# Kernel optimization log

Hardware: AMD Instinct MI355X
Metric: run time of the kernel (lower is better)

The kernel has to match this reference:

```python
import jax, jax.numpy as jnp
import numpy as np

LOW_RANK = 32      # low_rank_dim
N_CAND = 2048      # n_candidates
CHUNK = 128        # chunk_size
AUX_PCT = 0.2      # Settings.aux_loss_percent


def _normalize(x, eps=1e-12):
    # matches torch.nn.functional.normalize(p=2, dim=-1)
    n = jnp.linalg.norm(x, axis=-1, keepdims=True)
    return x / jnp.maximum(n, eps)


def setup_inputs() -> dict:
    key = jax.random.key(0)
    k1, k2, k3 = jax.random.split(key, 3)
    V, D, B, S = 50257, 1024, 4, 2048
    return {
        "hidden_states": jax.random.normal(k1, (B, S, D), jnp.float32),
        "embedding_weight": jax.random.normal(k2, (V, D), jnp.float32) * 0.02,
        "logit_scale": jnp.asarray(2.6592, jnp.float32),
        "target_ids": jax.random.randint(k3, (B, S), 0, V, dtype=jnp.int32),
    }


def reference(hidden_states, embedding_weight, logit_scale, target_ids):
    d = hidden_states.shape[-1]
    h = hidden_states.reshape(-1, d)            # [T, d]
    t = target_ids.reshape(-1)                  # [T]
    T = h.shape[0]
    n_chunks = T // CHUNK                       # T assumed divisible by CHUNK

    # no_grad low-rank table used only for candidate scan
    w_low_norm = jax.lax.stop_gradient(_normalize(embedding_weight[:, :LOW_RANK]))  # [V, L]
    h_low = _normalize(h[:, :LOW_RANK]).reshape(n_chunks, CHUNK, LOW_RANK)          # [n, C, L]
    h_full = _normalize(h).reshape(n_chunks, CHUNK, d)                              # [n, C, d]
    t_c = t.reshape(n_chunks, CHUNK)

    scale = 100.0 * jax.nn.sigmoid(logit_scale) + 1.0

    # with_batch_mean=True path: one scan per chunk using chunk-mean query (no_grad)
    h_mean = jax.lax.stop_gradient(h_low.mean(axis=1))      # [n, L]
    scan_logits = h_mean @ w_low_norm.T                     # [n, V]
    _, top_idx = jax.lax.top_k(scan_logits, N_CAND)         # [n, K]

    cand = embedding_weight[top_idx]                        # [n, K, d] (gather)
    cand_n = _normalize(cand)
    full_sims = jnp.einsum('ncd,nkd->nck', h_full, cand_n)  # [n, C, K]

    w_low_cand = _normalize(cand[..., :LOW_RANK])           # [n, K, L]
    low_sims = jnp.einsum('ncl,nkl->nck', h_low, w_low_cand)

    tgt_emb = embedding_weight[t_c]                         # [n, C, d]
    tgt_full_sim = jnp.sum(h_full * _normalize(tgt_emb), axis=-1)              # [n, C]
    tgt_low_sim = jnp.sum(h_low * _normalize(tgt_emb[..., :LOW_RANK]), axis=-1)

    is_tgt = top_idx[:, None, :] == t_c[:, :, None]         # [n, C, K]
    neg_inf = jnp.float32(-jnp.inf)

    # cross_entropy with label 0 == logsumexp(logits) - logits[..., 0]
    main_logits = jnp.concatenate(
        [tgt_full_sim[..., None] * scale,
         jnp.where(is_tgt, neg_inf, full_sims * scale)], axis=-1)
    main_loss = jnp.sum(jax.nn.logsumexp(main_logits, axis=-1) - main_logits[..., 0])

    aux_logits = jnp.concatenate(
        [tgt_low_sim[..., None] * scale,
         jnp.where(is_tgt, neg_inf, low_sims * scale)], axis=-1)
    aux_loss = jnp.sum(jax.nn.logsumexp(aux_logits, axis=-1) - aux_logits[..., 0])

    return (main_loss + AUX_PCT * aux_loss) / T
```

## Files before the change

### kernel.cpp

```cpp
#include <hip/hip_runtime.h>
#include <cstdint>
#include <cstddef>

#define V_SIZE 50257
#define V_PAD  50432
#define NV4    (V_PAD/4)
#define NVB    ((V_SIZE + 3) / 4)
#define D_DIM  1024
#define T_TOK  8192
#define NCHUNK 64
#define CCHUNK 128
#define NCAND  2048
#define LOWR   32
#define SDCAP  4096
#define ESCALE 32.0f

typedef unsigned int  uint32;
typedef unsigned short u16;
typedef unsigned char u8;
typedef unsigned long long u64;
typedef __attribute__((ext_vector_type(8))) short short8;
typedef __attribute__((ext_vector_type(4))) float f32x4;

__device__ __forceinline__ u16 f2bf(float f){
  uint32 u = __float_as_uint(f);
  return (u16)((u + 0x7FFFu + ((u >> 16) & 1u)) >> 16);
}
__device__ __forceinline__ uint32 key_of(float f){
  uint32 b = __float_as_uint(f);
  return b ^ ((uint32)((int)b >> 31) | 0x80000000u);
}
__device__ __forceinline__ int fxbin(float x){
  float c = fmaxf(fminf(x, 0.49f), -0.49f);
  int b = (int)(c * 4096.f) + 1024;
  return b < 0 ? 0 : (b > 2047 ? 2047 : b);
}
__device__ __forceinline__ float sigscale(const float* lsc){
  return 100.f / (1.f + __expf(-lsc[0])) + 1.f;
}
__device__ __forceinline__ float wred_sum(float v){
  #pragma unroll
  for (int m = 32; m >= 1; m >>= 1) v += __shfl_xor(v, m, 64);
  return v;
}
__device__ __forceinline__ float wred_max(float v){
  #pragma unroll
  for (int m = 32; m >= 1; m >>= 1) v = fmaxf(v, __shfl_xor(v, m, 64));
  return v;
}
__device__ __forceinline__ void gload_lds16(const void* g, void* l){
  __builtin_amdgcn_global_load_lds(
      (const __attribute__((address_space(1))) uint32*)g,
      (__attribute__((address_space(3))) uint32*)l, 16, 0, 0);
}
__device__ __forceinline__ void load_row16(const float* base, int lane, float* f){
  const float4* s4 = (const float4*)(base + lane * 16);
  float4 t0 = s4[0], t1 = s4[1], t2 = s4[2], t3 = s4[3];
  f[0]=t0.x; f[1]=t0.y; f[2]=t0.z;  f[3]=t0.w;
  f[4]=t1.x; f[5]=t1.y; f[6]=t1.z;  f[7]=t1.w;
  f[8]=t2.x; f[9]=t2.y; f[10]=t2.z; f[11]=t2.w;
  f[12]=t3.x; f[13]=t3.y; f[14]=t3.z; f[15]=t3.w;
}
__device__ __forceinline__ void store_bf16x16(u16* dst_base, int lane, const float* f){
  uint32 pk[8];
  #pragma unroll
  for (int i=0;i<8;++i) pk[i] = (uint32)f2bf(f[2*i]) | ((uint32)f2bf(f[2*i+1]) << 16);
  uint4* d = (uint4*)(dst_base + lane * 16);
  d[0] = make_uint4(pk[0],pk[1],pk[2],pk[3]);
  d[1] = make_uint4(pk[4],pk[5],pk[6],pk[7]);
}
__device__ __forceinline__ void store_fp8x16(u8* dst_base, int lane, const float* f, float sc){
  uint32 pk[4];
  #pragma unroll
  for (int i=0;i<4;++i){
    int w = __builtin_amdgcn_cvt_pk_fp8_f32(f[4*i]*sc,   f[4*i+1]*sc, 0, false);
    w     = __builtin_amdgcn_cvt_pk_fp8_f32(f[4*i+2]*sc, f[4*i+3]*sc, w, true);
    pk[i] = (uint32)w;
  }
  *(uint4*)(dst_base + lane * 16) = make_uint4(pk[0],pk[1],pk[2],pk[3]);
}
__device__ __forceinline__ int a8(int r, int slot8){
  return r*64 + ((((slot8>>1) ^ (r&3))) << 4) + ((slot8&1) << 3);
}

__global__ void __launch_bounds__(256)
prep_kernel(const float* __restrict__ emb, u8* __restrict__ emb8,
            u16* __restrict__ elow16,
            float* __restrict__ invn_f, float* __restrict__ invn_l,
            float* __restrict__ wlow,
            const float* __restrict__ h, u8* __restrict__ h8,
            u16* __restrict__ hlow16,
            float* __restrict__ invh_f, float* __restrict__ invh_l,
            float* __restrict__ hpart, uint32* __restrict__ ghist,
            float* __restrict__ out)
{
  const int bid = blockIdx.x;
  const int tid = threadIdx.x, lane = tid & 63, wid = tid >> 6;
  if (bid < NVB){
    if (bid == 0 && tid == 0) out[0] = 0.f;
    if (bid < 512 && tid < 64)
      ((uint4*)ghist)[bid * 64 + tid] = make_uint4(0,0,0,0);
    const int v = bid * 4 + wid;
    if (v >= V_SIZE) return;
    float f[16];
    load_row16(emb + (size_t)v * D_DIM, lane, f);
    float ss = 0.f;
    #pragma unroll
    for (int k=0;k<16;++k) ss += f[k]*f[k];
    float fullss = wred_sum(ss);
    float lowss  = wred_sum(lane < 2 ? ss : 0.f);
    store_fp8x16(emb8 + (size_t)v * D_DIM, lane, f, ESCALE);
    if (lane < 2){
      store_bf16x16(elow16 + (size_t)v * LOWR, lane, f);
      float4* wp = (float4*)(wlow + (size_t)v * LOWR + lane * 16);
      wp[0] = make_float4(f[0], f[1], f[2],  f[3]);
      wp[1] = make_float4(f[4], f[5], f[6],  f[7]);
      wp[2] = make_float4(f[8], f[9], f[10], f[11]);
      wp[3] = make_float4(f[12],f[13],f[14], f[15]);
    }
    if (lane == 0){
      invn_f[v] = 1.f / fmaxf(sqrtf(fullss), 1e-12f);
      invn_l[v] = 1.f / fmaxf(sqrtf(lowss),  1e-12f);
    }
    return;
  }
  const int bid2 = bid - NVB;
  const int nchunk = bid2 >> 3, sub = bid2 & 7;
  __shared__ float hm[LOWR];
  if (tid < LOWR) hm[tid] = 0.f;
  __syncthreads();
  for (int i = 0; i < 4; ++i){
    const int loc = sub*16 + wid*4 + i;
    const int tok = nchunk * CCHUNK + loc;
    float f[16];
    load_row16(h + (size_t)tok * D_DIM, lane, f);
    float ss = 0.f;
    #pragma unroll
    for (int k=0;k<16;++k) ss += f[k]*f[k];
    float fullss = wred_sum(ss);
    float lowss  = wred_sum(lane < 2 ? ss : 0.f);
    float invf = 1.f / fmaxf(sqrtf(fullss), 1e-12f);
    float invl = 1.f / fmaxf(sqrtf(lowss),  1e-12f);
    store_fp8x16(h8 + (size_t)tok * D_DIM, lane, f, 1.0f);
    if (lane < 2) store_bf16x16(hlow16 + (size_t)tok * LOWR, lane, f);
    if (lane == 0){ invh_f[tok] = invf; invh_l[tok] = invl; }
    if (lane < 2){
      #pragma unroll
      for (int k=0;k<16;++k) atomicAdd(&hm[lane*16 + k], f[k] * invl * (1.f/128.f));
    }
  }
  __syncthreads();
  if (tid < LOWR) hpart[(size_t)(nchunk*8 + sub) * LOWR + tid] = hm[tid];
}

__global__ void __launch_bounds__(256)
scan_kernel(const float* __restrict__ wlow, const float* __restrict__ invn_l,
            const float* __restrict__ hpart, float* __restrict__ scan)
{
  __shared__ float hm[NCHUNK * LOWR];
  for (int i = threadIdx.x; i < NCHUNK * LOWR; i += 256){
    const int nn = i >> 5, l = i & 31;
    float s = 0.f;
    #pragma unroll
    for (int p = 0; p < 8; ++p) s += hpart[(size_t)(nn*8 + p) * LOWR + l];
    hm[i] = s;
  }
  __syncthreads();
  const int v = blockIdx.x * 256 + threadIdx.x;
  if (v >= V_SIZE){
    if (v < V_PAD)
      for (int nn = 0; nn < NCHUNK; ++nn) scan[(size_t)nn * V_PAD + v] = -3.4e38f;
    return;
  }
  float w[LOWR];
  const float4* s4 = (const float4*)(wlow + (size_t)v * LOWR);
  #pragma unroll
  for (int i=0;i<8;++i){
    float4 t = s4[i];
    w[4*i]=t.x; w[4*i+1]=t.y; w[4*i+2]=t.z; w[4*i+3]=t.w;
  }
  const float inv = invn_l[v];
  #pragma unroll
  for (int i=0;i<LOWR;++i) w[i] *= inv;
  for (int nn = 0; nn < NCHUNK; ++nn){
    float d = 0.f;
    #pragma unroll
    for (int l=0;l<LOWR;++l) d += w[l] * hm[nn*LOWR + l];
    scan[(size_t)nn * V_PAD + v] = d;
  }
}

__global__ void __launch_bounds__(256)
topk_hist(const float* __restrict__ scan, uint32* __restrict__ ghist)
{
  const int nchunk = blockIdx.x, sub = blockIdx.y, tid = threadIdx.x;
  __shared__ uint32 hh[4][2048];
  for (int i = tid; i < 4*2048; i += 256) (&hh[0][0])[i] = 0;
  __syncthreads();
  const int cp = (tid >> 6) & 3;
  const float4* row = (const float4*)(scan + (size_t)nchunk * V_PAD) + sub * (NV4/8);
  for (int i = tid; i < NV4/8; i += 256){
    float4 x = row[i];
    atomicAdd(&hh[cp][fxbin(x.x)], 1u);
    atomicAdd(&hh[cp][fxbin(x.y)], 1u);
    atomicAdd(&hh[cp][fxbin(x.z)], 1u);
    atomicAdd(&hh[cp][fxbin(x.w)], 1u);
  }
  __syncthreads();
  uint32* gh = ghist + nchunk * 2048;
  for (int i = tid; i < 2048; i += 256){
    uint32 s = hh[0][i] + hh[1][i] + hh[2][i] + hh[3][i];
    if (s) atomicAdd(&gh[i], s);
  }
}

__global__ void __launch_bounds__(1024)
topk_select(const float* __restrict__ scan, const uint32* __restrict__ ghist,
            const float* __restrict__ invn_f, const float* __restrict__ invn_l,
            int* __restrict__ topidx, float* __restrict__ invc_f, float* __restrict__ invc_l)
{
  const int nchunk = blockIdx.x, tid = threadIdx.x, lane = tid & 63;
  __shared__ uint32 h[2048];
  __shared__ int gt_list[2048];
  __shared__ u64 sd_list[SDCAP];
  __shared__ uint32 rh[256];
  __shared__ uint32 n_gt, n_sd, s_tb, s_cgt, s_sel, s_cum, s_pos;
  if (tid == 0){ n_gt = 0; n_sd = 0; s_pos = 0; }
  for (int i = tid; i < 2048; i += 1024) h[i] = ghist[nchunk * 2048 + i];
  __syncthreads();
  if (tid < 64){
    uint32 c = 0;
    #pragma unroll 8
    for (int k = 0; k < 32; ++k) c += h[lane*32 + k];
    uint32 s = c;
    #pragma unroll
    for (int off = 1; off < 64; off <<= 1){
      uint32 t = __shfl_down(s, off, 64);
      if (lane + off < 64) s += t;
    }
    u64 m1 = __ballot(s >= NCAND);
    const int g = 63 - __builtin_clzll(m1);
    const uint32 cum = (g < 63) ? __shfl(s, g + 1, 64) : 0u;
    uint32 s2 = (lane < 32) ? h[g*32 + lane] : 0u;
    #pragma unroll
    for (int off = 1; off < 32; off <<= 1){
      uint32 t = __shfl_down(s2, off, 64);
      if (lane + off < 32) s2 += t;
    }
    u64 m2 = __ballot((lane < 32) && (cum + s2 >= NCAND));
    const int j = 63 - __builtin_clzll(m2);
    const uint32 cgt = cum + ((j < 31) ? __shfl(s2, j + 1, 64) : 0u);
    if (lane == 0){ s_tb = (uint32)(g*32 + j); s_cgt = cgt; }
  }
  __syncthreads();
  const int tb = (int)s_tb;
  const uint32 cgt = s_cgt;
  const float4* row = (const float4*)(scan + (size_t)nchunk * V_PAD);
  for (int i = tid; i < NV4; i += 1024){
    float4 x = row[i];
    const int vbase = i * 4;
    float vals[4] = {x.x, x.y, x.z, x.w};
    #pragma unroll
    for (int c = 0; c < 4; ++c){
      const int b = fxbin(vals[c]);
      const int v = vbase + c;
      const bool ok = (v < V_SIZE) && (b >= tb);
      const bool is_gt = ok && (b > tb);
      const bool is_sd = ok && (b == tb);
      const u64 mg = __ballot(is_gt);
      if (mg){
        const int ldr = (int)__builtin_ctzll(mg);
        uint32 base = 0;
        if (lane == ldr) base = atomicAdd(&n_gt, (uint32)__popcll(mg));
        base = __shfl(base, ldr, 64);
        if (is_gt){
          uint32 p = base + (uint32)__popcll(mg & ((1ull << lane) - 1ull));
          if (p < 2048u) gt_list[p] = v;
        }
      }
      const u64 ms = __ballot(is_sd);
      if (ms){
        const int ldr = (int)__builtin_ctzll(ms);
        uint32 base = 0;
        if (lane == ldr) base = atomicAdd(&n_sd, (uint32)__popcll(ms));
        base = __shfl(base, ldr, 64);
        if (is_sd){
          uint32 p = base + (uint32)__popcll(ms & ((1ull << lane) - 1ull));
          if (p < (uint32)SDCAP)
            sd_list[p] = ((u64)(~key_of(vals[c])) << 32) | (uint32)v;
        }
      }
    }
  }
  __syncthreads();
  const uint32 ng = n_gt < 2048u ? n_gt : 2048u;
  for (uint32 i = tid; i < ng; i += 1024){
    const int v = gt_list[i];
    const int o = nchunk * NCAND + (int)i;
    topidx[o] = v; invc_f[o] = invn_f[v]; invc_l[o] = invn_l[v];
  }
  const int n = (int)(n_sd < (uint32)SDCAP ? n_sd : (uint32)SDCAP);
  uint32 r = NCAND - cgt; if ((int)r > n) r = (uint32)n;
  u64 pref = 0;
  uint32 rem = r;
  const int bytes6[6] = {7,6,5,4,1,0};
  for (int bi = 0; bi < 6; ++bi){
    const int by = bytes6[bi];
    if (tid < 256) rh[tid] = 0;
    __syncthreads();
    const u64 pmask = (by == 7) ? 0ull : ((~0ull) << ((by+1)*8));
    for (int i = tid; i < n; i += 1024){
      u64 x = sd_list[i];
      if ((x & pmask) == pref) atomicAdd(&rh[(uint32)(x >> (by*8)) & 255u], 1u);
    }
    __syncthreads();
    if (tid < 64){
      const uint32 b0 = rh[lane*4], b1 = rh[lane*4+1], b2 = rh[lane*4+2], b3 = rh[lane*4+3];
      uint32 ps = b0 + b1 + b2 + b3;
      #pragma unroll
      for (int off = 1; off < 64; off <<= 1){
        uint32 t = __shfl_up(ps, off, 64);
        if (lane >= off) ps += t;
      }
      const u64 mm = __ballot(ps >= rem);
      const int gl = (int)__builtin_ctzll(mm);
      const uint32 before = (gl > 0) ? __shfl(ps, gl-1, 64) : 0u;
      if (lane == gl){
        uint32 cum = before; uint32 bsel = (uint32)gl * 4;
        if (cum + b0 < rem){ cum += b0; bsel++;
          if (cum + b1 < rem){ cum += b1; bsel++;
            if (cum + b2 < rem){ cum += b2; bsel++; } } }
        s_sel = bsel; s_cum = cum;
      }
    }
    __syncthreads();
    pref |= ((u64)s_sel) << (by*8);
    rem -= s_cum;
    __syncthreads();
  }
  for (int i = tid; i < n; i += 1024){
    u64 x = sd_list[i];
    if (x <= pref){
      uint32 p = atomicAdd(&s_pos, 1u);
      const int v = (int)(uint32)x;
      const int o = nchunk * NCAND + (int)(cgt + p);
      topidx[o] = v; invc_f[o] = invn_f[v]; invc_l[o] = invn_l[v];
    }
  }
}

__global__ void __launch_bounds__(256)
gemm_fused(const u8* __restrict__ h8, const u8* __restrict__ emb8,
           const u16* __restrict__ hlow16, const u16* __restrict__ elow16,
           const int* __restrict__ topidx,
           const float* __restrict__ invh_f, const float* __restrict__ invc_f,
           const float* __restrict__ invh_l, const float* __restrict__ invc_l,
           const int* __restrict__ tgts, const float* __restrict__ lsc,
           float* __restrict__ pm, float* __restrict__ pa)
{
  constexpr int NSTEP = 16;
  const int id = blockIdx.x;
  const int s_ = id >> 3;
  const int ntile = s_ & 31;
  const int nchunk = ((s_ >> 5) << 3) | (id & 7);
  const int tid = threadIdx.x, lane = tid & 63, wid = tid >> 6;
  const int wm = wid;
  const int fq = lane >> 4, fr = lane & 15;

  __shared__ u8 As[CCHUNK * 64];
  __shared__ u8 Bs[64 * 64];
  __shared__ float s_invh[CCHUNK], s_invhl[CCHUNK];
  __shared__ float s_invc[64], s_invcl[64];
  __shared__ int   s_tgt[CCHUNK], s_idx[64];

  if (tid < CCHUNK){
    s_invh[tid]  = invh_f[nchunk * CCHUNK + tid];
    s_invhl[tid] = invh_l[nchunk * CCHUNK + tid];
    s_tgt[tid]   = tgts[nchunk * CCHUNK + tid];
  }
  if (tid < 64){
    int o = nchunk * NCAND + ntile * 64 + tid;
    s_idx[tid]  = topidx[o];
    s_invc[tid] = invc_f[o];
    s_invcl[tid] = invc_l[o];
  }

  const int rl = lane >> 2;
  const int cbyte = ((lane & 3) ^ (rl & 3)) * 16;
  const char* aptr[2];
  const char* alptr[2];
  const char* bptr;
  const char* blptr;
  #pragma unroll
  for (int s = 0; s < 2; ++s){
    int row = wid * 32 + s * 16 + rl;
    aptr[s]  = (const char*)h8 + ((size_t)(nchunk * CCHUNK + row)) * D_DIM + cbyte;
    alptr[s] = (const char*)hlow16 + ((size_t)(nchunk * CCHUNK + row)) * (LOWR*2) + cbyte;
  }
  {
    int brow = wid * 16 + rl;
    int cidx = topidx[nchunk * NCAND + ntile * 64 + brow];
    bptr  = (const char*)emb8 + (size_t)cidx * D_DIM + cbyte;
    blptr = (const char*)elow16 + (size_t)cidx * (LOWR*2) + cbyte;
  }

  f32x4 acc[2][4];
  #pragma unroll
  for (int m=0;m<2;++m)
    #pragma unroll
    for (int q=0;q<4;++q)
      acc[m][q] = (f32x4){0.f,0.f,0.f,0.f};

  for (int st = 0; st < NSTEP; ++st){
    const int koff = st * 64;
    gload_lds16(aptr[0] + koff, (void*)&As[(wid*32 + 0 ) * 64]);
    gload_lds16(aptr[1] + koff, (void*)&As[(wid*32 + 16) * 64]);
    gload_lds16(bptr + koff,    (void*)&Bs[(wid*16) * 64]);
    __syncthreads();
    #pragma unroll
    for (int kk = 0; kk < 2; ++kk){
      long af[2], bf[4];
      #pragma unroll
      for (int m=0;m<2;++m)
        af[m] = *(const long*)&As[a8(wm*32 + m*16 + fr, kk*4 + fq)];
      #pragma unroll
      for (int q=0;q<4;++q)
        bf[q] = *(const long*)&Bs[a8(q*16 + fr, kk*4 + fq)];
      #pragma unroll
      for (int m=0;m<2;++m)
        #pragma unroll
        for (int q=0;q<4;++q)
          acc[m][q] = __builtin_amdgcn_mfma_f32_16x16x32_fp8_fp8(af[m], bf[q], acc[m][q], 0, 0, 0);
    }
    __syncthreads();
  }

  gload_lds16(alptr[0], (void*)&As[(wid*32 + 0 ) * 64]);
  gload_lds16(alptr[1], (void*)&As[(wid*32 + 16) * 64]);
  gload_lds16(blptr,    (void*)&Bs[(wid*16) * 64]);

  const float scale = sigscale(lsc);
  const float scm = scale * (1.0f / ESCALE);
  const float NEG = -__builtin_huge_valf();

  #pragma unroll
  for (int m=0;m<2;++m){
    #pragma unroll
    for (int j=0;j<4;++j){
      const int c = wm*32 + m*16 + fq*4 + j;
      const float ihs = s_invh[c] * scm;
      const int tg = s_tgt[c];
      float vals[4];
      #pragma unroll
      for (int q=0;q<4;++q){
        const int kl = q*16 + fr;
        float lg = acc[m][q][j] * ihs * s_invc[kl];
        vals[q] = (s_idx[kl] == tg) ? NEG : lg;
      }
      float lmax = fmaxf(fmaxf(vals[0], vals[1]), fmaxf(vals[2], vals[3]));
      #pragma unroll
      for (int ms=1; ms<16; ms<<=1) lmax = fmaxf(lmax, __shfl_xor(lmax, ms, 64));
      float se = 0.f;
      #pragma unroll
      for (int q=0;q<4;++q) se += __expf(vals[q] - lmax);
      #pragma unroll
      for (int ms=1; ms<16; ms<<=1) se += __shfl_xor(se, ms, 64);
      if (fr == 0){
        size_t pos = ((size_t)(nchunk*32 + ntile) * CCHUNK + c) * 2;
        pm[pos]   = lmax;
        pm[pos+1] = se;
      }
    }
  }

  __syncthreads();

  f32x4 acc2[2][4];
  {
    short8 afa[2], bfa[4];
    #pragma unroll
    for (int m=0;m<2;++m){
      const int r = wm*32 + m*16 + fr;
      afa[m] = *(const short8*)&As[r*64 + ((fq ^ (r & 3)) << 4)];
    }
    #pragma unroll
    for (int q=0;q<4;++q){
      const int r = q*16 + fr;
      bfa[q] = *(const short8*)&Bs[r*64 + ((fq ^ (r & 3)) << 4)];
    }
    #pragma unroll
    for (int m=0;m<2;++m)
      #pragma unroll
      for (int q=0;q<4;++q)
        acc2[m][q] = __builtin_amdgcn_mfma_f32_16x16x32_bf16(
            afa[m], bfa[q], (f32x4){0.f,0.f,0.f,0.f}, 0, 0, 0);
  }

  #pragma unroll
  for (int m=0;m<2;++m){
    #pragma unroll
    for (int j=0;j<4;++j){
      const int c = wm*32 + m*16 + fq*4 + j;
      const float ihs = s_invhl[c] * scale;
      const int tg = s_tgt[c];
      float vals[4];
      #pragma unroll
      for (int q=0;q<4;++q){
        const int kl = q*16 + fr;
        float lg = acc2[m][q][j] * ihs * s_invcl[kl];
        vals[q] = (s_idx[kl] == tg) ? NEG : lg;
      }
      float lmax = fmaxf(fmaxf(vals[0], vals[1]), fmaxf(vals[2], vals[3]));
      #pragma unroll
      for (int ms=1; ms<16; ms<<=1) lmax = fmaxf(lmax, __shfl_xor(lmax, ms, 64));
      float se = 0.f;
      #pragma unroll
      for (int q=0;q<4;++q) se += __expf(vals[q] - lmax);
      #pragma unroll
      for (int ms=1; ms<16; ms<<=1) se += __shfl_xor(se, ms, 64);
      if (fr == 0){
        size_t pos = ((size_t)(nchunk*32 + ntile) * CCHUNK + c) * 2;
        pa[pos]   = lmax;
        pa[pos+1] = se;
      }
    }
  }
}

__global__ void __launch_bounds__(256)
merge_loss(const float* __restrict__ h, const float* __restrict__ emb,
           const int* __restrict__ tgts,
           const float* __restrict__ invh_f, const float* __restrict__ invh_l,
           const float* __restrict__ invn_f, const float* __restrict__ invn_l,
           const float* __restrict__ pm, const float* __restrict__ pa,
           const float* __restrict__ lsc, float* __restrict__ out)
{
  const int nchunk = blockIdx.x >> 2, quarter = blockIdx.x & 3;
  const int tid = threadIdx.x, lane = tid & 63, wid = tid >> 6;
  const float scale = sigscale(lsc);
  const float NEG = -__builtin_huge_valf();
  float wacc = 0.f;
  for (int i = 0; i < 8; ++i){
    const int loc = quarter*32 + wid*8 + i;
    const int tok = nchunk * CCHUNK + loc;
    const int t = tgts[tok];
    float hf[16], ef[16];
    load_row16(h + (size_t)tok * D_DIM, lane, hf);
    load_row16(emb + (size_t)t * D_DIM, lane, ef);
    float part = 0.f;
    #pragma unroll
    for (int k=0;k<16;++k) part += hf[k]*ef[k];
    float dfull = wred_sum(part);
    float dlow  = wred_sum(lane < 2 ? part : 0.f);
    float tful = dfull * invh_f[tok] * invn_f[t] * scale;
    float tlow = dlow  * invh_l[tok] * invn_l[t] * scale;

    float mi = NEG, si = 0.f, mia = NEG, sia = 0.f;
    if (lane < 32){
      size_t q = ((size_t)(nchunk*32 + lane) * CCHUNK + loc) * 2;
      mi  = pm[q]; si  = pm[q+1];
      mia = pa[q]; sia = pa[q+1];
    }
    float M  = wred_max(mi);
    float S  = wred_sum(lane < 32 ? si * __expf(mi - M) : 0.f);
    float M2 = fmaxf(M, tful);
    float lmain = __logf(S * __expf(M - M2) + __expf(tful - M2)) + M2 - tful;
    float Ma  = wred_max(mia);
    float Sa  = wred_sum(lane < 32 ? sia * __expf(mia - Ma) : 0.f);
    float M2a = fmaxf(Ma, tlow);
    float laux = __logf(Sa * __expf(Ma - M2a) + __expf(tlow - M2a)) + M2a - tlow;
    wacc += lmain + 0.2f * laux;
  }
  __shared__ float ws4[4];
  if (lane == 0) ws4[wid] = wacc;
  __syncthreads();
  if (tid == 0) atomicAdd(out, (ws4[0]+ws4[1]+ws4[2]+ws4[3]) * (1.f / (float)T_TOK));
}

extern "C" void kernel_launch(void* const* d_in, const int* in_sizes, int n_in,
                              void* d_out, int out_size, void* d_ws, size_t ws_size,
                              hipStream_t stream)
{
  (void)in_sizes; (void)n_in; (void)out_size; (void)ws_size;
  const float* h   = (const float*)d_in[0];
  const float* emb = (const float*)d_in[1];
  const float* lsc = (const float*)d_in[2];
  const int*   tgt = (const int*)d_in[3];
  float* out = (float*)d_out;

  uint8_t* p = (uint8_t*)d_ws;
  auto carve = [&](size_t n)->uint8_t*{
    uint8_t* r = p; p += (n + 255) & ~(size_t)255; return r;
  };
  u8*    emb8   = (u8*)   carve((size_t)V_SIZE * D_DIM);
  u16*   elow16 = (u16*)  carve((size_t)V_SIZE * LOWR * 2);
  float* invn_f = (float*)carve((size_t)V_SIZE * 4);
  float* invn_l = (float*)carve((size_t)V_SIZE * 4);
  float* wlow   = (float*)carve((size_t)V_SIZE * LOWR * 4);
  u8*    h8     = (u8*)   carve((size_t)T_TOK * D_DIM);
  u16*   hlow16 = (u16*)  carve((size_t)T_TOK * LOWR * 2);
  float* invh_f = (float*)carve((size_t)T_TOK * 4);
  float* invh_l = (float*)carve((size_t)T_TOK * 4);
  float* hpart  = (float*)carve((size_t)NCHUNK * 8 * LOWR * 4);
  float* scan   = (float*)carve((size_t)NCHUNK * V_PAD * 4);
  uint32* ghist = (uint32*)carve((size_t)NCHUNK * 2048 * 4);
  int*   topidx = (int*)  carve((size_t)NCHUNK * NCAND * 4);
  float* invc_f = (float*)carve((size_t)NCHUNK * NCAND * 4);
  float* invc_l = (float*)carve((size_t)NCHUNK * NCAND * 4);
  float* pm     = (float*)carve((size_t)NCHUNK * 32 * CCHUNK * 2 * 4);
  float* pa     = (float*)carve((size_t)NCHUNK * 32 * CCHUNK * 2 * 4);

  prep_kernel<<<dim3(NVB + NCHUNK*8), dim3(256), 0, stream>>>(
      emb, emb8, elow16, invn_f, invn_l, wlow, h, h8, hlow16,
      invh_f, invh_l, hpart, ghist, out);
  scan_kernel<<<dim3(V_PAD / 256), dim3(256), 0, stream>>>(wlow, invn_l, hpart, scan);
  topk_hist<<<dim3(NCHUNK, 8), dim3(256), 0, stream>>>(scan, ghist);
  topk_select<<<dim3(NCHUNK), dim3(1024), 0, stream>>>(
      scan, ghist, invn_f, invn_l, topidx, invc_f, invc_l);
  gemm_fused<<<dim3(32 * NCHUNK), dim3(256), 0, stream>>>(
      h8, emb8, hlow16, elow16, topidx, invh_f, invc_f, invh_l, invc_l, tgt, lsc, pm, pa);
  merge_loss<<<dim3(NCHUNK * 4), dim3(256), 0, stream>>>(
      h, emb, tgt, invh_f, invh_l, invn_f, invn_l, pm, pa, lsc, out);
}
```

Baseline: 187.6 us.

## Fuse top-k histogram into select kernel and spread merge_loss over more blocks

Merges the separate histogram and selection kernels into a single per-chunk kernel that builds the bin histogram in shared memory. This removes the global histogram buffer, its zeroing in prep, the global atomics and one launch. The cost is that each chunk's histogram is now built by one 1024-thread block (64 blocks total) instead of 512 blocks, so there is less parallelism for that pass. merge_loss also goes from 256 to 1024 blocks, each handling 8 tokens, to raise occupancy at the price of more atomic adds to the output.

```diff
diff --git a/kernel.cpp b/kernel.cpp
--- a/kernel.cpp
+++ b/kernel.cpp
@@ -91,15 +91,12 @@
             const float* __restrict__ h, u8* __restrict__ h8,
             u16* __restrict__ hlow16,
             float* __restrict__ invh_f, float* __restrict__ invh_l,
-            float* __restrict__ hpart, uint32* __restrict__ ghist,
-            float* __restrict__ out)
+            float* __restrict__ hpart, float* __restrict__ out)
 {
   const int bid = blockIdx.x;
   const int tid = threadIdx.x, lane = tid & 63, wid = tid >> 6;
   if (bid < NVB){
     if (bid == 0 && tid == 0) out[0] = 0.f;
-    if (bid < 512 && tid < 64)
-      ((uint4*)ghist)[bid * 64 + tid] = make_uint4(0,0,0,0);
     const int v = bid * 4 + wid;
     if (v >= V_SIZE) return;
     float f[16];
@@ -190,16 +187,23 @@
   }
 }
 
-__global__ void __launch_bounds__(256)
-topk_hist(const float* __restrict__ scan, uint32* __restrict__ ghist)
+__global__ void __launch_bounds__(1024)
+topk_all(const float* __restrict__ scan,
+         const float* __restrict__ invn_f, const float* __restrict__ invn_l,
+         int* __restrict__ topidx, float* __restrict__ invc_f, float* __restrict__ invc_l)
 {
-  const int nchunk = blockIdx.x, sub = blockIdx.y, tid = threadIdx.x;
+  const int nchunk = blockIdx.x, tid = threadIdx.x, lane = tid & 63;
   __shared__ uint32 hh[4][2048];
-  for (int i = tid; i < 4*2048; i += 256) (&hh[0][0])[i] = 0;
-  __syncthreads();
+  __shared__ int gt_list[2048];
+  __shared__ u64 sd_list[SDCAP];
+  __shared__ uint32 rh[256];
+  __shared__ uint32 n_gt, n_sd, s_tb, s_cgt, s_sel, s_cum, s_pos;
+  if (tid == 0){ n_gt = 0; n_sd = 0; s_pos = 0; }
+  for (int i = tid; i < 4*2048; i += 1024) (&hh[0][0])[i] = 0;
+  __syncthreads();
+  const float4* row = (const float4*)(scan + (size_t)nchunk * V_PAD);
   const int cp = (tid >> 6) & 3;
-  const float4* row = (const float4*)(scan + (size_t)nchunk * V_PAD) + sub * (NV4/8);
-  for (int i = tid; i < NV4/8; i += 256){
+  for (int i = tid; i < NV4; i += 1024){
     float4 x = row[i];
     atomicAdd(&hh[cp][fxbin(x.x)], 1u);
     atomicAdd(&hh[cp][fxbin(x.y)], 1u);
@@ -207,31 +211,13 @@
     atomicAdd(&hh[cp][fxbin(x.w)], 1u);
   }
   __syncthreads();
-  uint32* gh = ghist + nchunk * 2048;
-  for (int i = tid; i < 2048; i += 256){
-    uint32 s = hh[0][i] + hh[1][i] + hh[2][i] + hh[3][i];
-    if (s) atomicAdd(&gh[i], s);
-  }
-}
-
-__global__ void __launch_bounds__(1024)
-topk_select(const float* __restrict__ scan, const uint32* __restrict__ ghist,
-            const float* __restrict__ invn_f, const float* __restrict__ invn_l,
-            int* __restrict__ topidx, float* __restrict__ invc_f, float* __restrict__ invc_l)
-{
-  const int nchunk = blockIdx.x, tid = threadIdx.x, lane = tid & 63;
-  __shared__ uint32 h[2048];
-  __shared__ int gt_list[2048];
-  __shared__ u64 sd_list[SDCAP];
-  __shared__ uint32 rh[256];
-  __shared__ uint32 n_gt, n_sd, s_tb, s_cgt, s_sel, s_cum, s_pos;
-  if (tid == 0){ n_gt = 0; n_sd = 0; s_pos = 0; }
-  for (int i = tid; i < 2048; i += 1024) h[i] = ghist[nchunk * 2048 + i];
+  for (int i = tid; i < 2048; i += 1024)
+    hh[0][i] = hh[0][i] + hh[1][i] + hh[2][i] + hh[3][i];
   __syncthreads();
   if (tid < 64){
     uint32 c = 0;
     #pragma unroll 8
-    for (int k = 0; k < 32; ++k) c += h[lane*32 + k];
+    for (int k = 0; k < 32; ++k) c += hh[0][lane*32 + k];
     uint32 s = c;
     #pragma unroll
     for (int off = 1; off < 64; off <<= 1){
@@ -241,7 +227,7 @@
     u64 m1 = __ballot(s >= NCAND);
     const int g = 63 - __builtin_clzll(m1);
     const uint32 cum = (g < 63) ? __shfl(s, g + 1, 64) : 0u;
-    uint32 s2 = (lane < 32) ? h[g*32 + lane] : 0u;
+    uint32 s2 = (lane < 32) ? hh[0][g*32 + lane] : 0u;
     #pragma unroll
     for (int off = 1; off < 32; off <<= 1){
       uint32 t = __shfl_down(s2, off, 64);
@@ -255,7 +241,6 @@
   __syncthreads();
   const int tb = (int)s_tb;
   const uint32 cgt = s_cgt;
-  const float4* row = (const float4*)(scan + (size_t)nchunk * V_PAD);
   for (int i = tid; i < NV4; i += 1024){
     float4 x = row[i];
     const int vbase = i * 4;
@@ -535,13 +520,13 @@
            const float* __restrict__ pm, const float* __restrict__ pa,
            const float* __restrict__ lsc, float* __restrict__ out)
 {
-  const int nchunk = blockIdx.x >> 2, quarter = blockIdx.x & 3;
+  const int nchunk = blockIdx.x >> 4, sixteenth = blockIdx.x & 15;
   const int tid = threadIdx.x, lane = tid & 63, wid = tid >> 6;
   const float scale = sigscale(lsc);
   const float NEG = -__builtin_huge_valf();
   float wacc = 0.f;
-  for (int i = 0; i < 8; ++i){
-    const int loc = quarter*32 + wid*8 + i;
+  for (int i = 0; i < 2; ++i){
+    const int loc = sixteenth*8 + wid*2 + i;
     const int tok = nchunk * CCHUNK + loc;
     const int t = tgts[tok];
     float hf[16], ef[16];
@@ -603,7 +588,6 @@
   float* invh_l = (float*)carve((size_t)T_TOK * 4);
   float* hpart  = (float*)carve((size_t)NCHUNK * 8 * LOWR * 4);
   float* scan   = (float*)carve((size_t)NCHUNK * V_PAD * 4);
-  uint32* ghist = (uint32*)carve((size_t)NCHUNK * 2048 * 4);
   int*   topidx = (int*)  carve((size_t)NCHUNK * NCAND * 4);
   float* invc_f = (float*)carve((size_t)NCHUNK * NCAND * 4);
   float* invc_l = (float*)carve((size_t)NCHUNK * NCAND * 4);
@@ -612,13 +596,12 @@
 
   prep_kernel<<<dim3(NVB + NCHUNK*8), dim3(256), 0, stream>>>(
       emb, emb8, elow16, invn_f, invn_l, wlow, h, h8, hlow16,
-      invh_f, invh_l, hpart, ghist, out);
+      invh_f, invh_l, hpart, out);
   scan_kernel<<<dim3(V_PAD / 256), dim3(256), 0, stream>>>(wlow, invn_l, hpart, scan);
-  topk_hist<<<dim3(NCHUNK, 8), dim3(256), 0, stream>>>(scan, ghist);
-  topk_select<<<dim3(NCHUNK), dim3(1024), 0, stream>>>(
-      scan, ghist, invn_f, invn_l, topidx, invc_f, invc_l);
+  topk_all<<<dim3(NCHUNK), dim3(1024), 0, stream>>>(
+      scan, invn_f, invn_l, topidx, invc_f, invc_l);
   gemm_fused<<<dim3(32 * NCHUNK), dim3(256), 0, stream>>>(
       h8, emb8, hlow16, elow16, topidx, invh_f, invc_f, invh_l, invc_l, tgt, lsc, pm, pa);
-  merge_loss<<<dim3(NCHUNK * 4), dim3(256), 0, stream>>>(
+  merge_loss<<<dim3(NCHUNK * 16), dim3(256), 0, stream>>>(
       h, emb, tgt, invh_f, invh_l, invn_f, invn_l, pm, pa, lsc, out);
 }
```

Result: slower. 192.7 us (+2.7%).
